# Optimization experiments

Measured on AMD Instinct MI355X. Metric: run time of the kernel, lower is better.

Reference implementation:

```python
import jax, jax.numpy as jnp
import numpy as np
import math

SQ, SK, B, NP, HN = 2048, 2048, 2, 16, 128
LAYER_NUM = 1  # coeff
NORM_FACTOR = math.sqrt(2048 / 16) * LAYER_NUM  # sqrt(HIDDEN/HEADS) * coeff
SCALE = float(LAYER_NUM)  # MLSASoftmax scale


def setup_inputs() -> dict:
    key = jax.random.key(0)
    kq, kk, kv = jax.random.split(key, 3)
    query_layer = jax.random.normal(kq, (SQ, B, NP, HN), dtype=jnp.float32)
    key_layer = jax.random.normal(kk, (SK, B, NP, HN), dtype=jnp.float32)
    value_layer = jax.random.normal(kv, (SK, B, NP, HN), dtype=jnp.float32)
    # Causal mask: True = masked, shape [b, 1, sq, sk] (broadcasts over heads)
    causal = jnp.triu(jnp.ones((SQ, SK), dtype=bool), k=1)
    attention_mask = jnp.broadcast_to(causal[None, None], (B, 1, SQ, SK))
    return {
        "query_layer": query_layer,
        "key_layer": key_layer,
        "value_layer": value_layer,
        "attention_mask": attention_mask,
    }


def reference(query_layer, key_layer, value_layer, attention_mask):
    # scores[b,n,s,t] = (Q . K) / norm_factor, then * coeff in softmax
    scores = jnp.einsum("sbnh,tbnh->bnst", query_layer, key_layer) / NORM_FACTOR
    scores = scores * SCALE
    scores = jnp.where(attention_mask, jnp.float32(-10000.0), scores)
    # Module computes exp/sum WITHOUT max-subtraction; replicate exactly.
    exp_mo = jnp.exp(scores)
    denomi = jnp.sum(exp_mo, axis=-1, keepdims=True)  # [b, np, sq, 1]
    probs = exp_mo / denomi
    # dropout is identity in eval / for deterministic baseline
    ctx = jnp.einsum("bnst,tbnh->sbnh", probs, value_layer)  # [sq, b, np, hn]
    sq, b, n, h = ctx.shape
    context_layer = ctx.reshape(sq, b, n * h)
    return (context_layer, denomi)
```

## Files before the change

kernel.cpp:

```cpp
#include <hip/hip_runtime.h>
#include <hip/hip_bf16.h>
#include <stdint.h>

typedef __attribute__((ext_vector_type(8))) short short8;
typedef __attribute__((ext_vector_type(8))) unsigned short ushort8;
typedef __attribute__((ext_vector_type(4))) float f32x4;
typedef __attribute__((ext_vector_type(4))) int int4v;

#define NHEAD 32
#define SEQ   2048
#define HN    128

static constexpr float INV_NORM = 0.08838834764831845f;

__device__ __forceinline__ unsigned short f2bf(float f) {
  union { float f; unsigned u; } v; v.f = f;
  unsigned r = v.u + 0x7fffu + ((v.u >> 16) & 1u);
  return (unsigned short)(r >> 16);
}

__device__ __forceinline__ f32x4 mfma16(short8 a, short8 b, f32x4 c) {
  return __builtin_amdgcn_mfma_f32_16x16x32_bf16(a, b, c, 0, 0, 0);
}

__device__ __forceinline__ void gl_lds16(const void* g, void* l) {
  __builtin_amdgcn_global_load_lds(
      (const __attribute__((address_space(1))) unsigned int*)g,
      (__attribute__((address_space(3))) unsigned int*)l, 16, 0, 0);
}

__global__ __launch_bounds__(256) void prep_kv(const float* __restrict__ K,
                                               const float* __restrict__ V,
                                               unsigned short* __restrict__ kfr,
                                               unsigned short* __restrict__ vfr) {
  __shared__ unsigned short lds[128 * 136];
  int bid = blockIdx.x;
  int tid = threadIdx.x;
  if (bid < 4096) {
    int idx = bid * 256 + tid;
    int cl = idx & 15;
    int t  = (idx >> 4) & 2047;
    int bn = idx >> 15;
    const float4* src = (const float4*)(K + ((size_t)t * 32 + bn) * 128 + cl * 8);
    float4 a = src[0], b = src[1];
    ushort8 o;
    o[0]=f2bf(a.x); o[1]=f2bf(a.y); o[2]=f2bf(a.z); o[3]=f2bf(a.w);
    o[4]=f2bf(b.x); o[5]=f2bf(b.y); o[6]=f2bf(b.z); o[7]=f2bf(b.w);
    int tile = t >> 5, r = t & 31;
    int nt = r >> 4, lr = r & 15;
    int kk = cl >> 2, hc = cl & 3;
    *(ushort8*)(kfr + (size_t)bn * 262144 + tile * 4096 +
                (nt * 4 + kk) * 512 + (hc * 16 + lr) * 8) = o;
  } else {
    int vb = bid - 4096;
    int bn = vb >> 4;
    int t0 = (vb & 15) << 7;
    int r = tid >> 1, h0 = (tid & 1) * 64;
    const float* src = V + ((size_t)(t0 + r) * 32 + bn) * 128 + h0;
#pragma unroll
    for (int j = 0; j < 8; ++j) {
      float4 a = *(const float4*)(src + j * 8);
      float4 b = *(const float4*)(src + j * 8 + 4);
      ushort8 o;
      o[0]=f2bf(a.x); o[1]=f2bf(a.y); o[2]=f2bf(a.z); o[3]=f2bf(a.w);
      o[4]=f2bf(b.x); o[5]=f2bf(b.y); o[6]=f2bf(b.z); o[7]=f2bf(b.w);
      *(ushort8*)&lds[r * 136 + h0 + j * 8] = o;
    }
    __syncthreads();
    int h = tid >> 1, ts = (tid & 1) * 64;
    unsigned short tmp[64];
#pragma unroll
    for (int j = 0; j < 64; ++j) {
      int p = j & 31;
      int tloc = ((p >> 3) & 3) * 4 + ((p >> 2) & 1) * 16 + (p & 3);
      tmp[j] = lds[(ts + (j & 32) + tloc) * 136 + h];
    }
#pragma unroll
    for (int j = 0; j < 8; ++j) {
      int c0 = t0 + ts + j * 8;
      int tg = c0 >> 5;
      int hv = (c0 >> 3) & 3;
      size_t du = (size_t)bn * 32768 + (size_t)tg * 512 +
                  (h >> 4) * 64 + hv * 16 + (h & 15);
      *(ushort8*)(vfr + du * 8) = *(ushort8*)&tmp[j * 8];
    }
  }
}

__device__ __forceinline__ short8 packp(const float (&e)[8], float& da) {
  da += ((e[0] + e[1]) + (e[2] + e[3])) + ((e[4] + e[5]) + (e[6] + e[7]));
  unsigned w0, w1, w2, w3;
  asm("v_cvt_pk_bf16_f32 %0, %1, %2" : "=v"(w0) : "v"(e[0]), "v"(e[1]));
  asm("v_cvt_pk_bf16_f32 %0, %1, %2" : "=v"(w1) : "v"(e[2]), "v"(e[3]));
  asm("v_cvt_pk_bf16_f32 %0, %1, %2" : "=v"(w2) : "v"(e[4]), "v"(e[5]));
  asm("v_cvt_pk_bf16_f32 %0, %1, %2" : "=v"(w3) : "v"(e[6]), "v"(e[7]));
  union { int4v u; short8 s; } pk;
  pk.u = (int4v){(int)w0, (int)w1, (int)w2, (int)w3};
  return pk.s;
}

__device__ __forceinline__ short8 softp_m(const f32x4 (&sv)[2], int t0h, int qbase,
                                          int l15, int hi, float& da) {
  float e[8];
#pragma unroll
  for (int nt = 0; nt < 2; ++nt)
#pragma unroll
    for (int i = 0; i < 4; ++i) {
      float x = __expf(sv[nt][i]);
      int kv = t0h + nt * 16 + hi * 4 + i;
      e[nt * 4 + i] = (kv <= qbase + l15) ? x : 0.0f;
    }
  return packp(e, da);
}

__device__ __forceinline__ short8 softp_u(const f32x4 (&sv)[2], float& da) {
  float e[8];
#pragma unroll
  for (int nt = 0; nt < 2; ++nt)
#pragma unroll
    for (int i = 0; i < 4; ++i)
      e[nt * 4 + i] = __expf(sv[nt][i]);
  return packp(e, da);
}

__global__ __launch_bounds__(512, 2) void attn_main(const float* __restrict__ Q,
                                                    const unsigned short* __restrict__ kfr,
                                                    const unsigned short* __restrict__ vfr,
                                                    float* __restrict__ out) {
  __shared__ char smem[65536];
  int tid = threadIdx.x;
  int lane = tid & 63;
  int w = tid >> 6;
  int l15 = lane & 15;
  int hi = lane >> 4;

  int bid = blockIdx.x;
  int bn = bid & 31;
  int z = bid >> 5;
  int qt = (z < 8) ? (15 - z) : (z - 8);
  int qb = qt * 128 + w * 16;
  int ntile = 2 * qt + 2;

  short8 qf[4];
  {
    const float* qrow = Q + ((size_t)(qb + l15) * 32 + bn) * 128;
#pragma unroll
    for (int kk = 0; kk < 4; ++kk) {
      float4 a = *(const float4*)(qrow + kk * 32 + hi * 8);
      float4 b = *(const float4*)(qrow + kk * 32 + hi * 8 + 4);
      short8 o;
      o[0]=(short)f2bf(a.x*INV_NORM); o[1]=(short)f2bf(a.y*INV_NORM);
      o[2]=(short)f2bf(a.z*INV_NORM); o[3]=(short)f2bf(a.w*INV_NORM);
      o[4]=(short)f2bf(b.x*INV_NORM); o[5]=(short)f2bf(b.y*INV_NORM);
      o[6]=(short)f2bf(b.z*INV_NORM); o[7]=(short)f2bf(b.w*INV_NORM);
      qf[kk] = o;
    }
  }

  f32x4 zz = {0.f, 0.f, 0.f, 0.f};
  f32x4 acc[8];
#pragma unroll
  for (int ht = 0; ht < 8; ++ht) acc[ht] = zz;
  float dacc = 0.f;

  const char* kg = (const char*)kfr + (size_t)bn * 524288;
  const char* vg = (const char*)vfr + (size_t)bn * 524288;

  auto stage = [&](int buf, int it) {
    const char* ks_ = kg + (size_t)it * 16384;
    char* kd = smem + buf * 16384;
    gl_lds16(ks_ + (size_t)tid * 16, kd + tid * 16);
    gl_lds16(ks_ + (size_t)(tid + 512) * 16, kd + (tid + 512) * 16);
    const char* vs_ = vg + (size_t)it * 16384;
    char* vd = smem + 32768 + buf * 16384;
    gl_lds16(vs_ + (size_t)tid * 16, vd + tid * 16);
    gl_lds16(vs_ + (size_t)(tid + 512) * 16, vd + (tid + 512) * 16);
  };

  asm volatile("s_waitcnt vmcnt(0)" ::: "memory");
  stage(0, 0);

  int cur = 0;
  for (int it = 0; it < ntile; ++it) {
    int t0 = it * 64;
    asm volatile("s_waitcnt vmcnt(0)" ::: "memory");
    __builtin_amdgcn_s_barrier();
    if (it + 1 < ntile) stage(cur ^ 1, it + 1);

    const char* kb = smem + cur * 16384;
    const char* vb = smem + 32768 + cur * 16384;
#pragma unroll
    for (int half = 0; half < 2; ++half) {
      int t0h = t0 + half * 32;
      if (t0h <= qb + 15) {
        const char* kbh = kb + half * 8192;
        const char* vbh = vb + half * 8192;
        short8 kf[2][4];
#pragma unroll
        for (int nt = 0; nt < 2; ++nt)
#pragma unroll
          for (int kk = 0; kk < 4; ++kk)
            kf[nt][kk] = *(const short8*)(kbh + ((nt * 4 + kk) * 64 + lane) * 16);
        f32x4 sv[2] = {zz, zz};
        __builtin_amdgcn_s_setprio(1);
#pragma unroll
        for (int nt = 0; nt < 2; ++nt)
#pragma unroll
          for (int kk = 0; kk < 4; ++kk)
            sv[nt] = mfma16(kf[nt][kk], qf[kk], sv[nt]);
        __builtin_amdgcn_s_setprio(0);
        short8 vf[8];
#pragma unroll
        for (int ht = 0; ht < 8; ++ht)
          vf[ht] = *(const short8*)(vbh + (ht * 64 + lane) * 16);
        bool mask = (t0h + 31 > qb);
        short8 p = mask ? softp_m(sv, t0h, qb, l15, hi, dacc)
                        : softp_u(sv, dacc);
        __builtin_amdgcn_s_setprio(1);
#pragma unroll
        for (int ht = 0; ht < 8; ++ht)
          acc[ht] = mfma16(p, vf[ht], acc[ht]);
        __builtin_amdgcn_s_setprio(0);
      }
    }
    cur ^= 1;
  }

  {
    float d = dacc;
    d += __shfl_xor(d, 16);
    d += __shfl_xor(d, 32);
    dacc = d;
  }
  float* dn = out + 8388608;
  if (hi == 0) dn[(size_t)bn * 2048 + qb + l15] = dacc;

  float inv[4];
#pragma unroll
  for (int i = 0; i < 4; ++i)
    inv[i] = __builtin_amdgcn_rcpf(__shfl(dacc, hi * 4 + i));

#pragma unroll
  for (int i = 0; i < 4; ++i) {
    float* orow = out + (size_t)(qb + hi * 4 + i) * 4096 + bn * 128 + l15;
#pragma unroll
    for (int ht = 0; ht < 8; ++ht)
      orow[ht * 16] = acc[ht][i] * inv[i];
  }
}

extern "C" void kernel_launch(void* const* d_in, const int* in_sizes, int n_in,
                              void* d_out, int out_size, void* d_ws, size_t ws_size,
                              hipStream_t stream) {
  const float* Q = (const float*)d_in[0];
  const float* K = (const float*)d_in[1];
  const float* V = (const float*)d_in[2];
  float* out = (float*)d_out;

  unsigned short* kfr = (unsigned short*)d_ws;
  unsigned short* vfr = kfr + (size_t)NHEAD * SEQ * HN;

  prep_kv<<<4608, 256, 0, stream>>>(K, V, kfr, vfr);
  attn_main<<<512, 512, 0, stream>>>(Q, kfr, vfr, out);
}
```

Measured before the change: 73.84 us.

## Read V fragments directly from global and stage K via registers

```diff
diff --git a/kernel.cpp b/kernel.cpp
--- a/kernel.cpp
+++ b/kernel.cpp
@@ -21,12 +21,6 @@
 
 __device__ __forceinline__ f32x4 mfma16(short8 a, short8 b, f32x4 c) {
   return __builtin_amdgcn_mfma_f32_16x16x32_bf16(a, b, c, 0, 0, 0);
-}
-
-__device__ __forceinline__ void gl_lds16(const void* g, void* l) {
-  __builtin_amdgcn_global_load_lds(
-      (const __attribute__((address_space(1))) unsigned int*)g,
-      (__attribute__((address_space(3))) unsigned int*)l, 16, 0, 0);
 }
 
 __global__ __launch_bounds__(256) void prep_kv(const float* __restrict__ K,
@@ -127,7 +121,7 @@
                                                     const unsigned short* __restrict__ kfr,
                                                     const unsigned short* __restrict__ vfr,
                                                     float* __restrict__ out) {
-  __shared__ char smem[65536];
+  __shared__ char smem[32768];
   int tid = threadIdx.x;
   int lane = tid & 63;
   int w = tid >> 6;
@@ -166,35 +160,37 @@
   const char* kg = (const char*)kfr + (size_t)bn * 524288;
   const char* vg = (const char*)vfr + (size_t)bn * 524288;
 
-  auto stage = [&](int buf, int it) {
-    const char* ks_ = kg + (size_t)it * 16384;
-    char* kd = smem + buf * 16384;
-    gl_lds16(ks_ + (size_t)tid * 16, kd + tid * 16);
-    gl_lds16(ks_ + (size_t)(tid + 512) * 16, kd + (tid + 512) * 16);
-    const char* vs_ = vg + (size_t)it * 16384;
-    char* vd = smem + 32768 + buf * 16384;
-    gl_lds16(vs_ + (size_t)tid * 16, vd + tid * 16);
-    gl_lds16(vs_ + (size_t)(tid + 512) * 16, vd + (tid + 512) * 16);
-  };
-
-  asm volatile("s_waitcnt vmcnt(0)" ::: "memory");
-  stage(0, 0);
+  {
+    ushort8 k0 = *(const ushort8*)(kg + (size_t)tid * 16);
+    ushort8 k1 = *(const ushort8*)(kg + (size_t)(tid + 512) * 16);
+    *(ushort8*)(smem + tid * 16) = k0;
+    *(ushort8*)(smem + (tid + 512) * 16) = k1;
+  }
 
   int cur = 0;
   for (int it = 0; it < ntile; ++it) {
     int t0 = it * 64;
-    asm volatile("s_waitcnt vmcnt(0)" ::: "memory");
-    __builtin_amdgcn_s_barrier();
-    if (it + 1 < ntile) stage(cur ^ 1, it + 1);
+    __syncthreads();
+
+    bool pre = (it + 1 < ntile);
+    ushort8 kn0, kn1;
+    if (pre) {
+      const char* ks = kg + (size_t)(it + 1) * 16384;
+      kn0 = *(const ushort8*)(ks + (size_t)tid * 16);
+      kn1 = *(const ushort8*)(ks + (size_t)(tid + 512) * 16);
+    }
 
     const char* kb = smem + cur * 16384;
-    const char* vb = smem + 32768 + cur * 16384;
 #pragma unroll
     for (int half = 0; half < 2; ++half) {
       int t0h = t0 + half * 32;
       if (t0h <= qb + 15) {
         const char* kbh = kb + half * 8192;
-        const char* vbh = vb + half * 8192;
+        const char* vbg = vg + (size_t)(it * 2 + half) * 8192;
+        short8 vf[8];
+#pragma unroll
+        for (int ht = 0; ht < 8; ++ht)
+          vf[ht] = *(const short8*)(vbg + ht * 1024 + lane * 16);
         short8 kf[2][4];
 #pragma unroll
         for (int nt = 0; nt < 2; ++nt)
@@ -209,10 +205,6 @@
           for (int kk = 0; kk < 4; ++kk)
             sv[nt] = mfma16(kf[nt][kk], qf[kk], sv[nt]);
         __builtin_amdgcn_s_setprio(0);
-        short8 vf[8];
-#pragma unroll
-        for (int ht = 0; ht < 8; ++ht)
-          vf[ht] = *(const short8*)(vbh + (ht * 64 + lane) * 16);
         bool mask = (t0h + 31 > qb);
         short8 p = mask ? softp_m(sv, t0h, qb, l15, hi, dacc)
                         : softp_u(sv, dacc);
@@ -222,6 +214,11 @@
           acc[ht] = mfma16(p, vf[ht], acc[ht]);
         __builtin_amdgcn_s_setprio(0);
       }
+    }
+    if (pre) {
+      char* kd = smem + (cur ^ 1) * 16384;
+      *(ushort8*)(kd + tid * 16) = kn0;
+      *(ushort8*)(kd + (tid + 512) * 16) = kn1;
     }
     cur ^= 1;
   }
```

After: 97.81 us. +32.5%, slower.
